# Kernel optimization log

Measured on AMD Instinct MI355X. Metric: run time of the kernel, lower is better.

Reference implementation:

```python
import jax, jax.numpy as jnp
import numpy as np

CAUSAL = True


def setup_inputs() -> dict:
    key = jax.random.key(0)
    k1, k2, k3 = jax.random.split(key, 3)
    B, S, D_IN, D_INNER, D_OUT = 4, 4096, 512, 64, 512
    x = jax.random.normal(k1, (B, S, D_IN), dtype=jnp.float32)
    W_qkv = jax.random.normal(k2, (D_IN, 3 * D_INNER), dtype=jnp.float32) * (D_IN ** -0.5)
    W_out = jax.random.normal(k3, (D_INNER, D_OUT), dtype=jnp.float32) * (D_INNER ** -0.5)
    b_out = jnp.zeros((D_OUT,), dtype=jnp.float32)
    return {"x": x, "W_qkv": W_qkv, "W_out": W_out, "b_out": b_out}


def reference(x, W_qkv, W_out, b_out):
    d_inner = W_out.shape[0]
    scale = d_inner ** -0.5
    qkv = jnp.einsum('bsi,io->bso', x, W_qkv)  # [B,S,3*d_inner]
    q, k, v = jnp.split(qkv, 3, axis=-1)
    sim = jnp.einsum('bid,bjd->bij', q, k) * scale  # [B,S,S]
    if CAUSAL:
        S = x.shape[1]
        mask = jnp.triu(jnp.ones((S, S), dtype=bool), k=1)
        sim = jnp.where(mask[None], -jnp.finfo(q.dtype).max, sim)
    attn = jax.nn.softmax(sim, axis=-1)
    out = jnp.einsum('bij,bjd->bid', attn, v)  # [B,S,d_inner]
    return jnp.einsum('bid,do->bio', out, W_out) + b_out
```

## Files before the change

### kernel.cpp

```cpp
#include <hip/hip_runtime.h>
#include <math.h>

typedef __attribute__((ext_vector_type(8))) short short8;
typedef __attribute__((ext_vector_type(4))) short short4v;
typedef __attribute__((ext_vector_type(4))) float f32x4;
typedef __attribute__((ext_vector_type(4))) float float4v;

__device__ __forceinline__ unsigned short f2bf(float f){
  unsigned int u = __float_as_uint(f);
  u += 0x7FFFu + ((u >> 16) & 1u);
  return (unsigned short)(u >> 16);
}
__device__ __forceinline__ float bf2f(short s){
  return __uint_as_float(((unsigned int)(unsigned short)s) << 16);
}

typedef __attribute__((address_space(1))) const unsigned char* gas_t;
typedef __attribute__((address_space(3))) unsigned char* las_t;
__device__ __forceinline__ void async16(const void* g, void* l) {
  __builtin_amdgcn_global_load_lds((gas_t)g, (las_t)l, 16, 0, 0);
}

#define SC2 0.1803368801111204f

__global__ __launch_bounds__(256) void prep_w(
    const float* __restrict__ Wqkv, const float* __restrict__ Wout,
    unsigned short* __restrict__ Wtq, unsigned short* __restrict__ Wto)
{
  int idx = blockIdx.x * 256 + threadIdx.x;
  if (idx < 192 * 512) {
    int n = idx >> 9, k = idx & 511;
    Wtq[idx] = f2bf(Wqkv[k * 192 + n]);
  } else {
    int i2 = idx - 192 * 512;
    int n = i2 >> 6, k = i2 & 63;
    Wto[i2] = f2bf(Wout[k * 512 + n]);
  }
}

__global__ __launch_bounds__(256) void qkv_kernel(
    const float* __restrict__ x,
    const unsigned short* __restrict__ Wt,
    unsigned short* __restrict__ qg,
    unsigned short* __restrict__ kg,
    unsigned short* __restrict__ vT)
{
  __shared__ __align__(16) unsigned short Wb[64][128];
  __shared__ __align__(16) unsigned short vbuf[64][72];
  const int part = blockIdx.x % 3;
  const int rb   = blockIdx.x / 3;
  const int lane = threadIdx.x & 63;
  const int wave = threadIdx.x >> 6;
  const int mrow = lane & 15;
  const int quad = lane >> 4;
  const int mb = rb * 64;
  const int m0 = mb + wave * 16;
  const int sw = mrow & 7;

  const int srow = lane >> 4;
  const int sch  = lane & 15;
#define STAGE_W(s)                                                            \
  {                                                                           \
    _Pragma("unroll")                                                         \
    for (int ii = 0; ii < 4; ii++) {                                          \
      const int r0 = wave * 16 + ii * 4;                                      \
      const int r  = r0 + srow;                                               \
      const int cd = (sch & 8) | ((sch ^ (r & 7)) & 7);                       \
      async16(Wt + (size_t)(part * 64 + r) * 512 + (s) * 128 + cd * 8,        \
              &Wb[r0][0]);                                                    \
    }                                                                         \
  }

  STAGE_W(0)

  f32x4 acc[4];
#pragma unroll
  for (int t = 0; t < 4; t++) acc[t] = (f32x4){0.f, 0.f, 0.f, 0.f};
  const float* xp = x + (size_t)(m0 + mrow) * 512 + quad * 8;

  for (int s = 0; s < 4; s++) {
    __syncthreads();
#pragma unroll
    for (int l = 0; l < 4; l++) {
      const int kk = s * 4 + l;
      float4v a0 = *(const float4v*)(xp + kk * 32);
      float4v a1 = *(const float4v*)(xp + kk * 32 + 4);
      short8 af;
#pragma unroll
      for (int j = 0; j < 4; j++) { af[j] = (short)f2bf(a0[j]); af[4 + j] = (short)f2bf(a1[j]); }
      const int c   = l * 4 + quad;
      const int pos = (c & 8) | ((c ^ sw) & 7);
#pragma unroll
      for (int t = 0; t < 4; t++) {
        short8 bf = *(const short8*)(&Wb[t * 16 + mrow][0] + pos * 8);
        acc[t] = __builtin_amdgcn_mfma_f32_16x16x32_bf16(af, bf, acc[t], 0, 0, 0);
      }
    }
    __syncthreads();
    if (s < 3) STAGE_W(s + 1)
  }

#pragma unroll
  for (int t = 0; t < 4; t++)
#pragma unroll
    for (int r = 0; r < 4; r++)
      vbuf[wave * 16 + quad * 4 + r][t * 16 + mrow] = f2bf(acc[t][r]);
  __syncthreads();

  if (part < 2) {
    unsigned short* dst = part ? kg : qg;
    const int row = threadIdx.x >> 2;
    const int seg = (threadIdx.x & 3) * 16;
    short8 w0 = *(const short8*)&vbuf[row][seg];
    short8 w1 = *(const short8*)&vbuf[row][seg + 8];
    unsigned short* p = dst + (size_t)(mb + row) * 64 + seg;
    *(short8*)(p) = w0;
    *(short8*)(p + 8) = w1;
  } else {
    const int d  = threadIdx.x >> 2;
    const int s8 = (threadIdx.x & 3) * 16;
    const int bb = rb >> 6;
    const int sb = mb & 4095;
    short8 w0, w1;
#pragma unroll
    for (int i = 0; i < 8; i++) {
      w0[i] = (short)vbuf[s8 + i][d];
      w1[i] = (short)vbuf[s8 + 8 + i][d];
    }
    unsigned short* dst = vT + (size_t)bb * (64 * 4096) + (size_t)d * 4096 + sb + s8;
    *(short8*)(dst) = w0;
    *(short8*)(dst + 8) = w1;
  }
#undef STAGE_W
}

template <bool MASKED>
__device__ __forceinline__ void soft_pv(
    const f32x4* sA, const short8* vf, int kb, int qlane, int quad, int mrow,
    float& lacc, f32x4* o, unsigned short (*pb)[72])
{
  float p[16];
#pragma unroll
  for (int t = 0; t < 4; t++)
#pragma unroll
    for (int r = 0; r < 4; r++) {
      float v = sA[t][r];
      if (MASKED && (kb + t * 16 + quad * 4 + r > qlane)) v = -3.0e38f;
      p[t * 4 + r] = exp2f(v * SC2);
    }
  float ps = 0.f;
#pragma unroll
  for (int i = 0; i < 16; i++) ps += p[i];
  lacc += ps;
#pragma unroll
  for (int t = 0; t < 4; t++) {
    short4v pk;
#pragma unroll
    for (int r = 0; r < 4; r++) pk[r] = (short)f2bf(p[t * 4 + r]);
    *(short4v*)&pb[mrow][t * 16 + quad * 4] = pk;
  }
  short8 pf0 = *(const short8*)&pb[mrow][quad * 8];
  short8 pf1 = *(const short8*)&pb[mrow][32 + quad * 8];
#pragma unroll
  for (int c = 0; c < 4; c++) {
    o[c] = __builtin_amdgcn_mfma_f32_16x16x32_bf16(vf[2 * c],     pf0, o[c], 0, 0, 0);
    o[c] = __builtin_amdgcn_mfma_f32_16x16x32_bf16(vf[2 * c + 1], pf1, o[c], 0, 0, 0);
  }
}

__global__ __launch_bounds__(256) void attn_kernel(
    const unsigned short* __restrict__ qg,
    const unsigned short* __restrict__ kg,
    const unsigned short* __restrict__ vT,
    unsigned short* __restrict__ Opart,
    float* __restrict__ lpart)
{
  __shared__ __align__(16) unsigned short Kb[2][64][64];
  __shared__ __align__(16) unsigned short Vb[2][64][64];
  __shared__ __align__(16) unsigned short pbuf[4][16][72];
  const int lane = threadIdx.x & 63;
  const int wave = threadIdx.x >> 6;
  const int mrow = lane & 15;
  const int quad = lane >> 4;
  const int sw   = mrow & 7;

  int t = 143 - (blockIdx.x % 144);
  const int b = blockIdx.x / 144;
  int qj = 31, c = 0;
  for (int qq = 0; qq < 32; qq++) {
    const int ncq = (qq >> 2) + 1;
    if (t < ncq) { qj = qq; c = t; break; }
    t -= ncq;
  }

  const int sq0w = qj * 128 + wave * 32;
  const int g0w  = b * 4096 + sq0w;

  short8 qf[2][2];
#pragma unroll
  for (int s = 0; s < 2; s++) {
    const unsigned short* qp = qg + (size_t)(g0w + 16 * s + mrow) * 64 + quad * 8;
    qf[s][0] = *(const short8*)(qp);
    qf[s][1] = *(const short8*)(qp + 32);
  }

  const int kstart = c << 9;
  const int qend   = qj * 128 + 128;
  const int kend   = (kstart + 512 < qend) ? (kstart + 512) : qend;
  const int nTb    = (kend - kstart) >> 6;

  f32x4 o[2][4];
#pragma unroll
  for (int s = 0; s < 2; s++)
#pragma unroll
    for (int ct = 0; ct < 4; ct++) o[s][ct] = (f32x4){0.f, 0.f, 0.f, 0.f};
  float lr[2] = {0.f, 0.f};

  const unsigned short* kbase = kg + (size_t)b * 4096 * 64;
  const unsigned short* vbase = vT + (size_t)b * 64 * 4096;
  const int shalf = lane >> 3;
  const int sch   = lane & 7;

#define STAGE_KV(kb, Kd, Vd)                                                  \
  {                                                                           \
    _Pragma("unroll")                                                         \
    for (int ii = 0; ii < 2; ii++) {                                          \
      const int r0 = wave * 16 + ii * 8;                                      \
      const int r  = r0 + shalf;                                              \
      const int cd = sch ^ (r & 7);                                           \
      async16(kbase + (size_t)((kb) + r) * 64 + cd * 8, (Kd) + r0 * 64);      \
      async16(vbase + (size_t)r * 4096 + (kb) + cd * 8, (Vd) + r0 * 64);      \
    }                                                                         \
  }

  STAGE_KV(kstart, &Kb[0][0][0], &Vb[0][0][0])
  __syncthreads();

  for (int j = 0; j < nTb; j++) {
    const int kb = kstart + 64 * j;
    if (j + 1 < nTb)
      STAGE_KV(kb + 64, &Kb[(j + 1) & 1][0][0], &Vb[(j + 1) & 1][0][0])
    const unsigned short* Kc = &Kb[j & 1][0][0];
    const unsigned short* Vc = &Vb[j & 1][0][0];

    short8 kf[8];
#pragma unroll
    for (int tt = 0; tt < 4; tt++) {
      const unsigned short* kr = Kc + (tt * 16 + mrow) * 64;
      kf[2 * tt]     = *(const short8*)(kr + (quad ^ sw) * 8);
      kf[2 * tt + 1] = *(const short8*)(kr + ((quad + 4) ^ sw) * 8);
    }
    f32x4 sA[2][4];
    bool act[2];
#pragma unroll
    for (int s = 0; s < 2; s++) {
      act[s] = (kb <= sq0w + 16 * s + 15);
      if (act[s]) {
#pragma unroll
        for (int tt = 0; tt < 4; tt++) {
          f32x4 z = (f32x4){0.f, 0.f, 0.f, 0.f};
          z = __builtin_amdgcn_mfma_f32_16x16x32_bf16(kf[2 * tt],     qf[s][0], z, 0, 0, 0);
          z = __builtin_amdgcn_mfma_f32_16x16x32_bf16(kf[2 * tt + 1], qf[s][1], z, 0, 0, 0);
          sA[s][tt] = z;
        }
      }
    }
    short8 vf[8];
#pragma unroll
    for (int cc = 0; cc < 4; cc++) {
      const unsigned short* vr = Vc + (cc * 16 + mrow) * 64;
      vf[2 * cc]     = *(const short8*)(vr + (quad ^ sw) * 8);
      vf[2 * cc + 1] = *(const short8*)(vr + ((quad + 4) ^ sw) * 8);
    }
#pragma unroll
    for (int s = 0; s < 2; s++) {
      if (!act[s]) continue;
      const int qlo = sq0w + 16 * s;
      if (kb + 63 <= qlo)
        soft_pv<false>(sA[s], vf, kb, qlo + mrow, quad, mrow, lr[s], o[s], pbuf[wave]);
      else
        soft_pv<true> (sA[s], vf, kb, qlo + mrow, quad, mrow, lr[s], o[s], pbuf[wave]);
    }
    __syncthreads();
  }
#undef STAGE_KV

#pragma unroll
  for (int s = 0; s < 2; s++) {
    float lt = lr[s];
    lt += __shfl_xor(lt, 16);
    lt += __shfl_xor(lt, 32);
    const size_t row = (size_t)c * 16384 + g0w + 16 * s + mrow;
#pragma unroll
    for (int ct = 0; ct < 4; ct++) {
      short4v ob;
#pragma unroll
      for (int r = 0; r < 4; r++) ob[r] = (short)f2bf(o[s][ct][r]);
      *(short4v*)(Opart + row * 64 + ct * 16 + quad * 4) = ob;
    }
    if (quad == 0) lpart[row] = lt;
  }
}

__global__ __launch_bounds__(256) void combine_kernel(
    const unsigned short* __restrict__ Opart,
    const float* __restrict__ lpart,
    const unsigned short* __restrict__ WtO,
    const float* __restrict__ bias,
    float* __restrict__ out)
{
  __shared__ __align__(16) unsigned short Wob[128][64];
  __shared__ __align__(16) float obuf[4][16][132];
  const int lane = threadIdx.x & 63;
  const int wave = threadIdx.x >> 6;
  const int mrow = lane & 15;
  const int quad = lane >> 4;
  const int rb = blockIdx.x >> 2;
  const int ch = blockIdx.x & 3;
  const int g0 = rb * 64 + wave * 16;
  const int nc = ((g0 & 4095) >> 9) + 1;

  {
    const int half = lane >> 3;
    const int chp  = lane & 7;
#pragma unroll
    for (int ii = 0; ii < 4; ii++) {
      const int r0 = wave * 32 + ii * 8;
      const int r  = r0 + half;
      const int cd = chp ^ (r & 7);
      async16(WtO + (size_t)(ch * 128 + r) * 64 + cd * 8, &Wob[r0][0]);
    }
  }

  float L = 0.f;
  f32x4 A0 = (f32x4){0,0,0,0}, A1 = A0, A2 = A0, A3 = A0;
  for (int cI = 0; cI < nc; cI++) {
    const size_t row = (size_t)cI * 16384 + g0 + mrow;
    L += lpart[row];
    const unsigned short* op = Opart + row * 64 + quad * 8;
    short8 x0 = *(const short8*)(op);
    short8 x1 = *(const short8*)(op + 32);
#pragma unroll
    for (int j = 0; j < 4; j++) {
      A0[j] += bf2f(x0[j]); A1[j] += bf2f(x0[4 + j]);
      A2[j] += bf2f(x1[j]); A3[j] += bf2f(x1[4 + j]);
    }
  }
  const float inv = 1.0f / L;
  short8 of0, of1;
#pragma unroll
  for (int i = 0; i < 4; i++) {
    of0[i]     = (short)f2bf(A0[i] * inv);
    of0[i + 4] = (short)f2bf(A1[i] * inv);
    of1[i]     = (short)f2bf(A2[i] * inv);
    of1[i + 4] = (short)f2bf(A3[i] * inv);
  }
  __syncthreads();

  const int sw = mrow & 7;
#pragma unroll
  for (int t = 0; t < 8; t++) {
    const int n = ch * 128 + t * 16 + mrow;
    const unsigned short* wr = &Wob[t * 16 + mrow][0];
    short8 w0 = *(const short8*)(wr + (quad ^ sw) * 8);
    short8 w1 = *(const short8*)(wr + ((quad + 4) ^ sw) * 8);
    f32x4 pr = (f32x4){0,0,0,0};
    pr = __builtin_amdgcn_mfma_f32_16x16x32_bf16(of0, w0, pr, 0, 0, 0);
    pr = __builtin_amdgcn_mfma_f32_16x16x32_bf16(of1, w1, pr, 0, 0, 0);
    const float bv = bias[n];
#pragma unroll
    for (int r = 0; r < 4; r++)
      obuf[wave][quad * 4 + r][t * 16 + mrow] = pr[r] + bv;
  }
#pragma unroll
  for (int j = 0; j < 4; j++) {
#pragma unroll
    for (int h = 0; h < 2; h++) {
      const int row = 4 * j + (lane >> 4);
      const int col = 4 * (lane & 15) + 64 * h;
      float4v v = *(const float4v*)&obuf[wave][row][col];
      *(float4v*)(out + (size_t)(g0 + row) * 512 + ch * 128 + col) = v;
    }
  }
}

extern "C" void kernel_launch(void* const* d_in, const int* in_sizes, int n_in,
                              void* d_out, int out_size, void* d_ws, size_t ws_size,
                              hipStream_t stream) {
  const float* x    = (const float*)d_in[0];
  const float* Wqkv = (const float*)d_in[1];
  const float* Wout = (const float*)d_in[2];
  const float* bout = (const float*)d_in[3];
  float* out = (float*)d_out;

  unsigned short* q   = (unsigned short*)d_ws;
  unsigned short* k   = q   + 16384 * 64;
  unsigned short* vT  = k   + 16384 * 64;
  unsigned short* Wtq = vT  + 4 * 64 * 4096;
  unsigned short* Wto = Wtq + 192 * 512;
  unsigned short* Opart = Wto + 512 * 64;
  float* lprt = (float*)(Opart + (size_t)8 * 16384 * 64);

  prep_w<<<512, 256, 0, stream>>>(Wqkv, Wout, Wtq, Wto);
  qkv_kernel<<<768, 256, 0, stream>>>(x, Wtq, q, k, vT);
  attn_kernel<<<576, 256, 0, stream>>>(q, k, vT, Opart, lprt);
  combine_kernel<<<1024, 256, 0, stream>>>(Opart, lprt, Wto, bout, out);
}
```

Baseline: 149.3 us.

## Fuse QKV projection parts per block and halve attention key chunk size

The QKV projection kernel now computes all three q/k/v outputs in one block over 64 rows, staging all 192 weight rows in shared memory and reusing each x tile across the three outputs. Before, three blocks each reloaded and reconverted the same x rows. The attention split-K chunk shrinks from 512 to 256 keys, which roughly doubles the grid to 1088 blocks for better load balance. In exchange the combine kernel must reduce twice as many partial outputs and the Opart workspace doubles.

```diff
diff --git a/kernel.cpp b/kernel.cpp
--- a/kernel.cpp
+++ b/kernel.cpp
@@ -45,93 +45,107 @@
     unsigned short* __restrict__ kg,
     unsigned short* __restrict__ vT)
 {
-  __shared__ __align__(16) unsigned short Wb[64][128];
-  __shared__ __align__(16) unsigned short vbuf[64][72];
-  const int part = blockIdx.x % 3;
-  const int rb   = blockIdx.x / 3;
+  __shared__ __align__(16) unsigned short Wb[192][128];
   const int lane = threadIdx.x & 63;
   const int wave = threadIdx.x >> 6;
   const int mrow = lane & 15;
   const int quad = lane >> 4;
-  const int mb = rb * 64;
-  const int m0 = mb + wave * 16;
+  const int mb = blockIdx.x * 64;
   const int sw = mrow & 7;
 
-  const int srow = lane >> 4;
-  const int sch  = lane & 15;
+  const int lrow = lane >> 4;
+  const int lch  = lane & 15;
 #define STAGE_W(s)                                                            \
-  {                                                                           \
-    _Pragma("unroll")                                                         \
-    for (int ii = 0; ii < 4; ii++) {                                          \
-      const int r0 = wave * 16 + ii * 4;                                      \
-      const int r  = r0 + srow;                                               \
-      const int cd = (sch & 8) | ((sch ^ (r & 7)) & 7);                       \
-      async16(Wt + (size_t)(part * 64 + r) * 512 + (s) * 128 + cd * 8,        \
-              &Wb[r0][0]);                                                    \
-    }                                                                         \
-  }
+  { _Pragma("unroll")                                                         \
+    for (int i = 0; i < 12; i++) {                                            \
+      const int r0 = 4 * (wave * 12 + i);                                     \
+      const int r  = r0 + lrow;                                               \
+      const int cd = (lch & 8) | ((lch ^ (r & 7)) & 7);                       \
+      async16(Wt + (size_t)r * 512 + (s) * 128 + cd * 8, &Wb[r0][0]);         \
+    } }
 
   STAGE_W(0)
 
-  f32x4 acc[4];
-#pragma unroll
-  for (int t = 0; t < 4; t++) acc[t] = (f32x4){0.f, 0.f, 0.f, 0.f};
-  const float* xp = x + (size_t)(m0 + mrow) * 512 + quad * 8;
+  f32x4 acc[4][3];
+#pragma unroll
+  for (int rt = 0; rt < 4; rt++)
+#pragma unroll
+    for (int ct = 0; ct < 3; ct++) acc[rt][ct] = (f32x4){0.f, 0.f, 0.f, 0.f};
 
   for (int s = 0; s < 4; s++) {
     __syncthreads();
 #pragma unroll
-    for (int l = 0; l < 4; l++) {
-      const int kk = s * 4 + l;
-      float4v a0 = *(const float4v*)(xp + kk * 32);
-      float4v a1 = *(const float4v*)(xp + kk * 32 + 4);
-      short8 af;
-#pragma unroll
-      for (int j = 0; j < 4; j++) { af[j] = (short)f2bf(a0[j]); af[4 + j] = (short)f2bf(a1[j]); }
-      const int c   = l * 4 + quad;
+    for (int kkl = 0; kkl < 4; kkl++) {
+      short8 af[4];
+#pragma unroll
+      for (int rt = 0; rt < 4; rt++) {
+        const float* xp = x + (size_t)(mb + rt * 16 + mrow) * 512
+                            + s * 128 + kkl * 32 + quad * 8;
+        float4v a0 = *(const float4v*)(xp);
+        float4v a1 = *(const float4v*)(xp + 4);
+#pragma unroll
+        for (int j = 0; j < 4; j++) {
+          af[rt][j]     = (short)f2bf(a0[j]);
+          af[rt][4 + j] = (short)f2bf(a1[j]);
+        }
+      }
+      const int c   = kkl * 4 + quad;
       const int pos = (c & 8) | ((c ^ sw) & 7);
 #pragma unroll
-      for (int t = 0; t < 4; t++) {
-        short8 bf = *(const short8*)(&Wb[t * 16 + mrow][0] + pos * 8);
-        acc[t] = __builtin_amdgcn_mfma_f32_16x16x32_bf16(af, bf, acc[t], 0, 0, 0);
+      for (int ct = 0; ct < 3; ct++) {
+        short8 bf = *(const short8*)(&Wb[(wave * 3 + ct) * 16 + mrow][0] + pos * 8);
+#pragma unroll
+        for (int rt = 0; rt < 4; rt++)
+          acc[rt][ct] = __builtin_amdgcn_mfma_f32_16x16x32_bf16(af[rt], bf, acc[rt][ct], 0, 0, 0);
       }
     }
     __syncthreads();
     if (s < 3) STAGE_W(s + 1)
   }
-
-#pragma unroll
-  for (int t = 0; t < 4; t++)
-#pragma unroll
-    for (int r = 0; r < 4; r++)
-      vbuf[wave * 16 + quad * 4 + r][t * 16 + mrow] = f2bf(acc[t][r]);
+#undef STAGE_W
+
+  unsigned short* cb = &Wb[0][0];
+#pragma unroll
+  for (int rt = 0; rt < 4; rt++)
+#pragma unroll
+    for (int ct = 0; ct < 3; ct++)
+#pragma unroll
+      for (int r = 0; r < 4; r++)
+        cb[(rt * 16 + quad * 4 + r) * 200 + wave * 48 + ct * 16 + mrow] =
+            f2bf(acc[rt][ct][r]);
   __syncthreads();
 
-  if (part < 2) {
-    unsigned short* dst = part ? kg : qg;
-    const int row = threadIdx.x >> 2;
-    const int seg = (threadIdx.x & 3) * 16;
-    short8 w0 = *(const short8*)&vbuf[row][seg];
-    short8 w1 = *(const short8*)&vbuf[row][seg + 8];
-    unsigned short* p = dst + (size_t)(mb + row) * 64 + seg;
+  const int row = threadIdx.x >> 2;
+  const int seg = (threadIdx.x & 3) * 16;
+  {
+    short8 w0 = *(const short8*)&cb[row * 200 + seg];
+    short8 w1 = *(const short8*)&cb[row * 200 + seg + 8];
+    unsigned short* p = qg + (size_t)(mb + row) * 64 + seg;
     *(short8*)(p) = w0;
     *(short8*)(p + 8) = w1;
-  } else {
+  }
+  {
+    short8 w0 = *(const short8*)&cb[row * 200 + 64 + seg];
+    short8 w1 = *(const short8*)&cb[row * 200 + 64 + seg + 8];
+    unsigned short* p = kg + (size_t)(mb + row) * 64 + seg;
+    *(short8*)(p) = w0;
+    *(short8*)(p + 8) = w1;
+  }
+  {
     const int d  = threadIdx.x >> 2;
     const int s8 = (threadIdx.x & 3) * 16;
-    const int bb = rb >> 6;
+    const int bb = blockIdx.x >> 6;
     const int sb = mb & 4095;
     short8 w0, w1;
 #pragma unroll
     for (int i = 0; i < 8; i++) {
-      w0[i] = (short)vbuf[s8 + i][d];
-      w1[i] = (short)vbuf[s8 + 8 + i][d];
+      w0[i] = (short)cb[(s8 + i) * 200 + 128 + d];
+      w1[i] = (short)cb[(s8 + 8 + i) * 200 + 128 + d];
     }
     unsigned short* dst = vT + (size_t)bb * (64 * 4096) + (size_t)d * 4096 + sb + s8;
     *(short8*)(dst) = w0;
     *(short8*)(dst + 8) = w1;
   }
-#undef STAGE_W
 }
 
 template <bool MASKED>
@@ -184,11 +198,11 @@
   const int quad = lane >> 4;
   const int sw   = mrow & 7;
 
-  int t = 143 - (blockIdx.x % 144);
-  const int b = blockIdx.x / 144;
+  int t = 271 - (blockIdx.x % 272);
+  const int b = blockIdx.x / 272;
   int qj = 31, c = 0;
   for (int qq = 0; qq < 32; qq++) {
-    const int ncq = (qq >> 2) + 1;
+    const int ncq = (qq >> 1) + 1;
     if (t < ncq) { qj = qq; c = t; break; }
     t -= ncq;
   }
@@ -204,9 +218,9 @@
     qf[s][1] = *(const short8*)(qp + 32);
   }
 
-  const int kstart = c << 9;
+  const int kstart = c << 8;
   const int qend   = qj * 128 + 128;
-  const int kend   = (kstart + 512 < qend) ? (kstart + 512) : qend;
+  const int kend   = (kstart + 256 < qend) ? (kstart + 256) : qend;
   const int nTb    = (kend - kstart) >> 6;
 
   f32x4 o[2][4];
@@ -318,7 +332,7 @@
   const int rb = blockIdx.x >> 2;
   const int ch = blockIdx.x & 3;
   const int g0 = rb * 64 + wave * 16;
-  const int nc = ((g0 & 4095) >> 9) + 1;
+  const int nc = ((g0 & 4095) >> 8) + 1;
 
   {
     const int half = lane >> 3;
@@ -399,10 +413,10 @@
   unsigned short* Wtq = vT  + 4 * 64 * 4096;
   unsigned short* Wto = Wtq + 192 * 512;
   unsigned short* Opart = Wto + 512 * 64;
-  float* lprt = (float*)(Opart + (size_t)8 * 16384 * 64);
+  float* lprt = (float*)(Opart + (size_t)16 * 16384 * 64);
 
   prep_w<<<512, 256, 0, stream>>>(Wqkv, Wout, Wtq, Wto);
-  qkv_kernel<<<768, 256, 0, stream>>>(x, Wtq, q, k, vT);
-  attn_kernel<<<576, 256, 0, stream>>>(q, k, vT, Opart, lprt);
+  qkv_kernel<<<256, 256, 0, stream>>>(x, Wtq, q, k, vT);
+  attn_kernel<<<1088, 256, 0, stream>>>(q, k, vT, Opart, lprt);
   combine_kernel<<<1024, 256, 0, stream>>>(Opart, lprt, Wto, bout, out);
 }
```

New measurement: 155.3 us. 1.04x slower.
